# Kernel tuning notes

Measured on AMD Instinct MI355X. Metric: run time of the kernel, lower is better.

## Reference

```python
import jax, jax.numpy as jnp
import numpy as np

N = 4096  # n == m: vector length and circulant size


def setup_inputs() -> dict:
    key = jax.random.key(0)
    ks = jax.random.split(key, 6)
    return {
        "key": jax.random.normal(ks[0], (N,), dtype=jnp.float32),
        "input_x": jax.random.normal(ks[1], (N,), dtype=jnp.float32),
        "key_matrix1": jax.random.normal(ks[2], (N, N), dtype=jnp.float32),
        "input_o1": jax.random.normal(ks[3], (N,), dtype=jnp.float32),
        "key_matrix2": jax.random.normal(ks[4], (N, N), dtype=jnp.float32),
        "input_o2": jax.random.normal(ks[5], (N,), dtype=jnp.float32),
    }


def reference(key, input_x, key_matrix1, input_o1, key_matrix2, input_o2):
    # Original loop: key_current_j[k] = key[(k - j) % m]  (a rolled copy of key),
    # result[j] = dot(key_current_j, input_x), then per-j correction:
    #   redun1 = (km1 @ key_current_j)[j]
    #   redun2 = sum_{i != j} (km1 @ key_current_j)[i] * input_o1[i]
    # and likewise redun3/redun4 with km2/input_o2; finally
    #   result[j] = (result[j] - redun2 - redun4) / redun1, returning (result, last redun3).
    n = input_x.shape[0]
    m = key.shape[0]
    # Circulant gather: K[j, k] = key[(k - j) % m], shape (n, m)
    idx = (jnp.arange(m)[None, :] - jnp.arange(n)[:, None]) % m
    K = key[idx]

    base = K @ input_x                                   # result before correction, (n,)

    # Diagonals of R = K @ km.T without forming R: d[j] = dot(K[j], km[j])
    d1 = jnp.einsum("jk,jk->j", K, key_matrix1)          # redun1 per j
    d2 = jnp.einsum("jk,jk->j", K, key_matrix2)          # redun3 per j

    # R @ o = (K @ km.T) @ o = K @ (km.T @ o): O(n^2) instead of O(n^3)
    r2 = K @ (key_matrix1.T @ input_o1) - d1 * input_o1  # redun2 per j (index j excluded)
    r4 = K @ (key_matrix2.T @ input_o2) - d2 * input_o2  # redun4 per j

    result = (base - r2 - r4) / d1
    redun3 = d2[-1]  # value from the last loop iteration j = n-1
    return result, redun3
```

## Files before the change

kernel.cpp:

```cpp
#include <hip/hip_runtime.h>

#define N 4096
#define MASK 4095

__device__ __forceinline__ float red32(float v) {
    v += __shfl_xor(v, 1, 64);
    v += __shfl_xor(v, 2, 64);
    v += __shfl_xor(v, 4, 64);
    v += __shfl_xor(v, 8, 64);
    v += __shfl_xor(v, 16, 64);
    return v;
}

__device__ __forceinline__ float fold(float u, float v, int m) {
    const bool hi = (threadIdx.x & m) != 0;
    const float t = hi ? u : v;
    const float s = __shfl_xor(t, m, 64);
    return (hi ? v : u) + s;
}

__device__ __forceinline__ float greduce4(float g0, float g1, float g2, float g3) {
    float c1 = fold(g0, g1, 32);
    float c2 = fold(g2, g3, 32);
    float e  = fold(c1, c2, 16);
    e += __shfl_xor(e, 8, 64);
    e += __shfl_xor(e, 4, 64);
    e += __shfl_xor(e, 2, 64);
    e += __shfl_xor(e, 1, 64);
    return e;
}

__global__ __launch_bounds__(256) void k1_fused(
    const float* __restrict__ key,
    const float* __restrict__ km1, const float* __restrict__ km2,
    const float* __restrict__ o1, const float* __restrict__ o2,
    float* __restrict__ tpart1, float* __restrict__ tpart2,
    float* __restrict__ dpart1, float* __restrict__ dpart2)
{
    __shared__ float sdp[8][8];
    const int t = threadIdx.x;
    const int b = blockIdx.x;
    const int mat = b >> 11;
    const int bb = b & 2047;
    const int rc = bb >> 2;
    const int cs = bb & 3;
    const int j0 = rc * 8;
    const int c0 = cs * 1024;

    const float* __restrict__ km = mat ? km2 : km1;
    const float* __restrict__ o  = mat ? o2  : o1;
    float* __restrict__ tp_out   = mat ? tpart2 : tpart1;
    float* __restrict__ dp_out   = mat ? dpart2 : dpart1;

    float w[11];
    #pragma unroll
    for (int i = 0; i < 11; ++i)
        w[i] = key[(c0 + 4 * t - j0 - 7 + i) & MASK];

    const float4* q = (const float4*)km + (size_t)j0 * 1024 + cs * 256 + t;

    float dpa[8];
    float tp[4] = {0.f, 0.f, 0.f, 0.f};

    #pragma unroll
    for (int rb = 0; rb < 2; ++rb) {
        float4 A[4];
        #pragma unroll
        for (int i = 0; i < 4; ++i) A[i] = q[(size_t)(rb * 4 + i) * 1024];
        #pragma unroll
        for (int rr = 0; rr < 4; ++rr) {
            const int r = rb * 4 + rr;
            const float4 a = A[rr];
            const float oa = o[j0 + r];
            tp[0] += oa * a.x; tp[1] += oa * a.y; tp[2] += oa * a.z; tp[3] += oa * a.w;
            dpa[r] = w[7 - r] * a.x + w[8 - r] * a.y + w[9 - r] * a.z + w[10 - r] * a.w;
        }
    }

    ((float4*)(tp_out + (size_t)rc * N + c0))[t] = make_float4(tp[0], tp[1], tp[2], tp[3]);

    const int hw = t >> 5;
    #pragma unroll
    for (int r = 0; r < 8; ++r) {
        const float v = red32(dpa[r]);
        if ((t & 31) == 0) sdp[r][hw] = v;
    }
    __syncthreads();

    if (t < 64) {
        const int g = t >> 3;
        const int s = t & 7;
        float v = sdp[g][s];
        v += __shfl_xor(v, 1, 64);
        v += __shfl_xor(v, 2, 64);
        v += __shfl_xor(v, 4, 64);
        if (s == 0) dp_out[(size_t)(j0 + g) * 4 + cs] = v;
    }
}

__global__ __launch_bounds__(256) void k2_reduce(
    const float* __restrict__ tpart1, const float* __restrict__ tpart2,
    const float* __restrict__ dpart1, const float* __restrict__ dpart2,
    float* __restrict__ t1, float* __restrict__ t2,
    float* __restrict__ d1, float* __restrict__ d2)
{
    __shared__ float sdata[256];
    const int b = blockIdx.x;
    const int t = threadIdx.x;

    if (b < 256) {
        const float* src = (b < 128) ? tpart1 : tpart2;
        float* dst       = (b < 128) ? t1 : t2;
        const int colbase = (b & 127) * 32;
        const int col = t & 31;
        const int sg = t >> 5;
        float a0 = 0.f, a1 = 0.f, a2 = 0.f, a3 = 0.f;
        #pragma unroll 4
        for (int k = 0; k < 64; k += 4) {
            a0 += src[(size_t)(sg + 8 * (k + 0)) * N + colbase + col];
            a1 += src[(size_t)(sg + 8 * (k + 1)) * N + colbase + col];
            a2 += src[(size_t)(sg + 8 * (k + 2)) * N + colbase + col];
            a3 += src[(size_t)(sg + 8 * (k + 3)) * N + colbase + col];
        }
        sdata[t] = (a0 + a1) + (a2 + a3);
        __syncthreads();
        if (t < 32) {
            float s = 0.f;
            #pragma unroll
            for (int i = 0; i < 8; ++i) s += sdata[i * 32 + t];
            dst[colbase + t] = s;
        }
    } else {
        const int row = (b - 256) * 256 + t;
        const float4 v1 = ((const float4*)dpart1)[row];
        const float4 v2 = ((const float4*)dpart2)[row];
        d1[row] = (v1.x + v1.y) + (v1.z + v1.w);
        d2[row] = (v2.x + v2.y) + (v2.z + v2.w);
    }
}

__global__ __launch_bounds__(256) void k3_final(
    const float* __restrict__ key, const float* __restrict__ x,
    const float* __restrict__ t1, const float* __restrict__ t2,
    const float* __restrict__ d1, const float* __restrict__ d2,
    const float* __restrict__ o1, const float* __restrict__ o2,
    float* __restrict__ out)
{
    __shared__ float skey[4096 + 128];
    __shared__ float sred[48];
    const int t = threadIdx.x;
    const int j0 = blockIdx.x * 4;

    #pragma unroll
    for (int q = 0; q < 16; ++q) {
        const int idx = q * 256 + t;
        skey[idx + (idx >> 5)] = key[idx];
    }
    __syncthreads();

    float acc[4][3];
    #pragma unroll
    for (int r = 0; r < 4; ++r)
        #pragma unroll
        for (int v = 0; v < 3; ++v) acc[r][v] = 0.f;

    #pragma unroll
    for (int q = 0; q < 4; ++q) {
        const int k0 = q * 1024 + 4 * t;
        const float4 xv = *(const float4*)(x + k0);
        const float4 u1 = *(const float4*)(t1 + k0);
        const float4 u2 = *(const float4*)(t2 + k0);
        float kw[7];
        #pragma unroll
        for (int i = 0; i < 7; ++i) {
            const int widx = (k0 - j0 - 3 + i) & MASK;
            kw[i] = skey[widx + (widx >> 5)];
        }
        #pragma unroll
        for (int r = 0; r < 4; ++r) {
            const float kv0 = kw[3 - r], kv1 = kw[4 - r], kv2 = kw[5 - r], kv3 = kw[6 - r];
            acc[r][0] += kv0 * xv.x + kv1 * xv.y + kv2 * xv.z + kv3 * xv.w;
            acc[r][1] += kv0 * u1.x + kv1 * u1.y + kv2 * u1.z + kv3 * u1.w;
            acc[r][2] += kv0 * u2.x + kv1 * u2.y + kv2 * u2.z + kv3 * u2.w;
        }
    }

    float rv[3];
    #pragma unroll
    for (int v = 0; v < 3; ++v)
        rv[v] = greduce4(acc[0][v], acc[1][v], acc[2][v], acc[3][v]);

    const int lane = t & 63, wave = t >> 6, sg = lane >> 4;
    const int off = (0x3120 >> (sg * 4)) & 0xF;
    if ((lane & 15) == 0) {
        #pragma unroll
        for (int v = 0; v < 3; ++v) sred[wave * 12 + v * 4 + off] = rv[v];
    }
    __syncthreads();

    if (t < 4) {
        const int j = j0 + t;
        float vb = 0.f, v1 = 0.f, v2 = 0.f;
        #pragma unroll
        for (int wv = 0; wv < 4; ++wv) {
            vb += sred[wv * 12 + 0 + t];
            v1 += sred[wv * 12 + 4 + t];
            v2 += sred[wv * 12 + 8 + t];
        }
        const float dd1 = d1[j], dd2 = d2[j];
        const float r2 = v1 - dd1 * o1[j];
        const float r4 = v2 - dd2 * o2[j];
        out[j] = (vb - r2 - r4) / dd1;
        if (j == N - 1) out[N] = dd2;
    }
}

extern "C" void kernel_launch(void* const* d_in, const int* in_sizes, int n_in,
                              void* d_out, int out_size, void* d_ws, size_t ws_size,
                              hipStream_t stream) {
    const float* key = (const float*)d_in[0];
    const float* x   = (const float*)d_in[1];
    const float* km1 = (const float*)d_in[2];
    const float* o1  = (const float*)d_in[3];
    const float* km2 = (const float*)d_in[4];
    const float* o2  = (const float*)d_in[5];
    float* out = (float*)d_out;

    float* ws = (float*)d_ws;
    float* tpart1 = ws;
    float* tpart2 = tpart1 + (size_t)512 * N;
    float* dpart1 = tpart2 + (size_t)512 * N;
    float* dpart2 = dpart1 + (size_t)N * 4;
    float* t1     = dpart2 + (size_t)N * 4;
    float* t2     = t1 + N;
    float* d1     = t2 + N;
    float* d2     = d1 + N;

    hipLaunchKernelGGL(k1_fused, dim3(4096), dim3(256), 0, stream,
                       key, km1, km2, o1, o2, tpart1, tpart2, dpart1, dpart2);
    hipLaunchKernelGGL(k2_reduce, dim3(272), dim3(256), 0, stream,
                       tpart1, tpart2, dpart1, dpart2, t1, t2, d1, d2);
    hipLaunchKernelGGL(k3_final, dim3(1024), dim3(256), 0, stream,
                       key, x, t1, t2, d1, d2, o1, o2, out);
}
```

Baseline: 38.31 us.

## Enlarge k1 tiles to 16 rows by 2048 columns, halving row-partial traffic

The first kernel now processes 16 rows and 2048 columns per block (1024 blocks instead of 4096), with each thread handling 8 columns. The key vector is staged in padded shared memory rather than gathered from global memory. Row-sum partials for t are halved (256 instead of 512 per matrix), which shrinks the intermediate traffic that k2 reads. Diagonal partials are written per half-wave without the shared-memory second stage, giving 16 partials per row that k2 now sums. Costs are fewer blocks for latency hiding, more registers per thread, and a per-block shared-memory fill of the key.

```diff
diff --git a/kernel.cpp b/kernel.cpp
--- a/kernel.cpp
+++ b/kernel.cpp
@@ -37,65 +37,84 @@
     float* __restrict__ tpart1, float* __restrict__ tpart2,
     float* __restrict__ dpart1, float* __restrict__ dpart2)
 {
-    __shared__ float sdp[8][8];
+    __shared__ float skey[4096 + 128];
     const int t = threadIdx.x;
     const int b = blockIdx.x;
-    const int mat = b >> 11;
-    const int bb = b & 2047;
-    const int rc = bb >> 2;
-    const int cs = bb & 3;
-    const int j0 = rc * 8;
-    const int c0 = cs * 1024;
+    const int mat = b >> 9;
+    const int sub = b & 511;
+    const int rc = sub >> 1;
+    const int cs = sub & 1;
+    const int j0 = rc * 16;
+    const int c0 = cs * 2048;
 
     const float* __restrict__ km = mat ? km2 : km1;
     const float* __restrict__ o  = mat ? o2  : o1;
     float* __restrict__ tp_out   = mat ? tpart2 : tpart1;
     float* __restrict__ dp_out   = mat ? dpart2 : dpart1;
 
-    float w[11];
-    #pragma unroll
-    for (int i = 0; i < 11; ++i)
-        w[i] = key[(c0 + 4 * t - j0 - 7 + i) & MASK];
-
-    const float4* q = (const float4*)km + (size_t)j0 * 1024 + cs * 256 + t;
-
-    float dpa[8];
-    float tp[4] = {0.f, 0.f, 0.f, 0.f};
-
-    #pragma unroll
-    for (int rb = 0; rb < 2; ++rb) {
-        float4 A[4];
-        #pragma unroll
-        for (int i = 0; i < 4; ++i) A[i] = q[(size_t)(rb * 4 + i) * 1024];
-        #pragma unroll
-        for (int rr = 0; rr < 4; ++rr) {
-            const int r = rb * 4 + rr;
-            const float4 a = A[rr];
-            const float oa = o[j0 + r];
-            tp[0] += oa * a.x; tp[1] += oa * a.y; tp[2] += oa * a.z; tp[3] += oa * a.w;
-            dpa[r] = w[7 - r] * a.x + w[8 - r] * a.y + w[9 - r] * a.z + w[10 - r] * a.w;
-        }
-    }
-
-    ((float4*)(tp_out + (size_t)rc * N + c0))[t] = make_float4(tp[0], tp[1], tp[2], tp[3]);
-
+    #pragma unroll
+    for (int q = 0; q < 4; ++q) {
+        const float4 kv = ((const float4*)key)[q * 256 + t];
+        const int idx = (q * 256 + t) * 4;
+        skey[(idx + 0) + ((idx + 0) >> 5)] = kv.x;
+        skey[(idx + 1) + ((idx + 1) >> 5)] = kv.y;
+        skey[(idx + 2) + ((idx + 2) >> 5)] = kv.z;
+        skey[(idx + 3) + ((idx + 3) >> 5)] = kv.w;
+    }
+    __syncthreads();
+
+    const int col0 = c0 + 8 * t;
+    const float4* qp = (const float4*)km + (size_t)j0 * 1024 + (c0 >> 2) + 2 * t;
     const int hw = t >> 5;
-    #pragma unroll
-    for (int r = 0; r < 8; ++r) {
-        const float v = red32(dpa[r]);
-        if ((t & 31) == 0) sdp[r][hw] = v;
-    }
-    __syncthreads();
-
-    if (t < 64) {
-        const int g = t >> 3;
-        const int s = t & 7;
-        float v = sdp[g][s];
-        v += __shfl_xor(v, 1, 64);
-        v += __shfl_xor(v, 2, 64);
-        v += __shfl_xor(v, 4, 64);
-        if (s == 0) dp_out[(size_t)(j0 + g) * 4 + cs] = v;
-    }
+
+    float tp[8];
+    #pragma unroll
+    for (int i = 0; i < 8; ++i) tp[i] = 0.f;
+
+    for (int h = 0; h < 2; ++h) {
+        const int jbase = j0 + 8 * h;
+        const float4* qh = qp + (size_t)h * 8 * 1024;
+
+        float w[15];
+        #pragma unroll
+        for (int i = 0; i < 15; ++i) {
+            const int idx = (col0 - jbase - 7 + i) & MASK;
+            w[i] = skey[idx + (idx >> 5)];
+        }
+
+        float dpa[8];
+        #pragma unroll
+        for (int rb = 0; rb < 4; ++rb) {
+            const int r0 = 2 * rb, r1 = 2 * rb + 1;
+            const float4 a0 = qh[(size_t)r0 * 1024];
+            const float4 b0 = qh[(size_t)r0 * 1024 + 1];
+            const float4 a1 = qh[(size_t)r1 * 1024];
+            const float4 b1 = qh[(size_t)r1 * 1024 + 1];
+            const float oa0 = o[jbase + r0];
+            const float oa1 = o[jbase + r1];
+
+            tp[0] += oa0 * a0.x; tp[1] += oa0 * a0.y; tp[2] += oa0 * a0.z; tp[3] += oa0 * a0.w;
+            tp[4] += oa0 * b0.x; tp[5] += oa0 * b0.y; tp[6] += oa0 * b0.z; tp[7] += oa0 * b0.w;
+            dpa[r0] = w[7 - r0] * a0.x + w[8 - r0] * a0.y + w[9 - r0] * a0.z + w[10 - r0] * a0.w
+                    + w[11 - r0] * b0.x + w[12 - r0] * b0.y + w[13 - r0] * b0.z + w[14 - r0] * b0.w;
+
+            tp[0] += oa1 * a1.x; tp[1] += oa1 * a1.y; tp[2] += oa1 * a1.z; tp[3] += oa1 * a1.w;
+            tp[4] += oa1 * b1.x; tp[5] += oa1 * b1.y; tp[6] += oa1 * b1.z; tp[7] += oa1 * b1.w;
+            dpa[r1] = w[7 - r1] * a1.x + w[8 - r1] * a1.y + w[9 - r1] * a1.z + w[10 - r1] * a1.w
+                    + w[11 - r1] * b1.x + w[12 - r1] * b1.y + w[13 - r1] * b1.z + w[14 - r1] * b1.w;
+        }
+
+        #pragma unroll
+        for (int r = 0; r < 8; ++r) {
+            const float v = red32(dpa[r]);
+            if ((t & 31) == 0)
+                dp_out[(size_t)(jbase + r) * 16 + cs * 8 + hw] = v;
+        }
+    }
+
+    float4* tpo = (float4*)(tp_out + (size_t)rc * N + c0) + 2 * t;
+    tpo[0] = make_float4(tp[0], tp[1], tp[2], tp[3]);
+    tpo[1] = make_float4(tp[4], tp[5], tp[6], tp[7]);
 }
 
 __global__ __launch_bounds__(256) void k2_reduce(
@@ -116,7 +135,7 @@
         const int sg = t >> 5;
         float a0 = 0.f, a1 = 0.f, a2 = 0.f, a3 = 0.f;
         #pragma unroll 4
-        for (int k = 0; k < 64; k += 4) {
+        for (int k = 0; k < 32; k += 4) {
             a0 += src[(size_t)(sg + 8 * (k + 0)) * N + colbase + col];
             a1 += src[(size_t)(sg + 8 * (k + 1)) * N + colbase + col];
             a2 += src[(size_t)(sg + 8 * (k + 2)) * N + colbase + col];
@@ -132,10 +151,18 @@
         }
     } else {
         const int row = (b - 256) * 256 + t;
-        const float4 v1 = ((const float4*)dpart1)[row];
-        const float4 v2 = ((const float4*)dpart2)[row];
-        d1[row] = (v1.x + v1.y) + (v1.z + v1.w);
-        d2[row] = (v2.x + v2.y) + (v2.z + v2.w);
+        const float4* p1 = (const float4*)(dpart1 + (size_t)row * 16);
+        const float4* p2 = (const float4*)(dpart2 + (size_t)row * 16);
+        float s1 = 0.f, s2 = 0.f;
+        #pragma unroll
+        for (int i = 0; i < 4; ++i) {
+            const float4 v1 = p1[i];
+            const float4 v2 = p2[i];
+            s1 += (v1.x + v1.y) + (v1.z + v1.w);
+            s2 += (v2.x + v2.y) + (v2.z + v2.w);
+        }
+        d1[row] = s1;
+        d2[row] = s2;
     }
 }
 
@@ -228,15 +255,15 @@
 
     float* ws = (float*)d_ws;
     float* tpart1 = ws;
-    float* tpart2 = tpart1 + (size_t)512 * N;
-    float* dpart1 = tpart2 + (size_t)512 * N;
-    float* dpart2 = dpart1 + (size_t)N * 4;
-    float* t1     = dpart2 + (size_t)N * 4;
+    float* tpart2 = tpart1 + (size_t)256 * N;
+    float* dpart1 = tpart2 + (size_t)256 * N;
+    float* dpart2 = dpart1 + (size_t)N * 16;
+    float* t1     = dpart2 + (size_t)N * 16;
     float* t2     = t1 + N;
     float* d1     = t2 + N;
     float* d2     = d1 + N;
 
-    hipLaunchKernelGGL(k1_fused, dim3(4096), dim3(256), 0, stream,
+    hipLaunchKernelGGL(k1_fused, dim3(1024), dim3(256), 0, stream,
                        key, km1, km2, o1, o2, tpart1, tpart2, dpart1, dpart2);
     hipLaunchKernelGGL(k2_reduce, dim3(272), dim3(256), 0, stream,
                        tpart1, tpart2, dpart1, dpart2, t1, t2, d1, d2);
```

Result: faster. 37.47 us (-2.2%).
